# Optimization experiments

Measured on AMD Instinct MI355X. Metric: run time of the kernel, lower is better.

## Reference

```python
import jax, jax.numpy as jnp
import numpy as np

N_QUBITS = 6

def _apply_1q(state, U, w):
    # state: [B] + [2]*6 complex; U: [2,2] complex
    ax = 1 + w
    s = jnp.moveaxis(state, ax, -1)
    s = jnp.einsum('...j,ij->...i', s, U)
    return jnp.moveaxis(s, -1, ax)

def _apply_cnot(state, ctrl, tgt):
    ca, ta = 1 + ctrl, 1 + tgt
    s = jnp.moveaxis(state, (ca, ta), (1, 2))  # [B,2,2,...]
    s = jnp.stack([s[:, 0], s[:, 1, ::-1]], axis=1)
    return jnp.moveaxis(s, (1, 2), (ca, ta))

def _rot(phi, theta, omega):
    # PennyLane Rot = RZ(omega) RY(theta) RZ(phi)
    c, s = jnp.cos(theta / 2), jnp.sin(theta / 2)
    return jnp.stack([
        jnp.stack([jnp.exp(-0.5j * (phi + omega)) * c, -jnp.exp(0.5j * (phi - omega)) * s]),
        jnp.stack([jnp.exp(-0.5j * (phi - omega)) * s, jnp.exp(0.5j * (phi + omega)) * c]),
    ])

def _quantum(xq, qw):
    B = xq.shape[0]
    # AngleEmbedding RY: product state, per-qubit amplitudes [cos(x/2), sin(x/2)]
    amps = jnp.stack([jnp.cos(xq / 2), jnp.sin(xq / 2)], axis=-1)  # [B,6,2]
    state = amps[:, 0]
    for i in range(1, N_QUBITS):
        state = jnp.einsum('b...,bj->b...j', state, amps[:, i])
    state = state.astype(jnp.complex64)  # [B,2,2,2,2,2,2]
    # StronglyEntanglingLayers: per layer Rot on each wire, then CNOT ring of range r
    n_layers = qw.shape[0]
    for l in range(n_layers):
        for w in range(N_QUBITS):
            U = _rot(qw[l, w, 0], qw[l, w, 1], qw[l, w, 2])
            state = _apply_1q(state, U, w)
        r = (l % (N_QUBITS - 1)) + 1  # default ranges
        for w in range(N_QUBITS):
            state = _apply_cnot(state, w, (w + r) % N_QUBITS)
    probs = jnp.abs(state) ** 2
    zs = []
    for w in range(N_QUBITS):
        axes = tuple(a for a in range(1, N_QUBITS + 1) if a != 1 + w)
        p = jnp.sum(probs, axis=axes)  # [B,2]
        zs.append(p[:, 0] - p[:, 1])
    return jnp.stack(zs, axis=-1)  # [B,6]

def setup_inputs() -> dict:
    key = jax.random.key(0)
    ks = jax.random.split(key, 10)
    B = 16384
    return {
        'xc': jax.random.normal(ks[0], (B, 2048), jnp.float32),
        'xq': jax.random.uniform(ks[1], (B, N_QUBITS), jnp.float32),
        'W1': jax.random.normal(ks[2], (64, 2048), jnp.float32) * 0.02,
        'b1': jnp.zeros((64,), jnp.float32),
        'qw': jax.random.uniform(ks[3], (3, N_QUBITS, 3), jnp.float32, 0.0, 2 * np.pi),
        'Wq': jax.random.normal(ks[4], (16, N_QUBITS), jnp.float32) * 0.3,
        'bq': jnp.zeros((16,), jnp.float32),
        'Wf': jax.random.normal(ks[5], (3, 80), jnp.float32) * 0.1,
        'bf': jnp.zeros((3,), jnp.float32),
    }

def reference(xc, xq, W1, b1, qw, Wq, bq, Wf, bf):
    c = jax.nn.relu(xc @ W1.T + b1)                 # [B,64]
    q = _quantum(xq, qw) @ Wq.T + bq                # [B,16]
    return jnp.concatenate([c, q], axis=1) @ Wf.T + bf  # [B,3]
```

## Files before the change

### kernel.cpp

```cpp
#include <hip/hip_runtime.h>
#include <hip/hip_bf16.h>

#define NQ 6

typedef __attribute__((ext_vector_type(8))) short short8;
typedef __attribute__((ext_vector_type(4))) float floatx4;

#define WS_MQ_F   8192
#define WS_CQ_F   (8192+18)
#define WS_W1BF_B 36864

typedef const __attribute__((address_space(1))) void gvoid_t;
typedef __attribute__((address_space(3))) void lvoid_t;

__global__ __launch_bounds__(64) void prep_kernel(
    const float* __restrict__ qw, int n_layers,
    const float* __restrict__ W1, const float* __restrict__ Wq,
    const float* __restrict__ bq, const float* __restrict__ Wf,
    const float* __restrict__ bf, float* __restrict__ ws_f,
    short* __restrict__ w1bf)
{
    const int blk  = blockIdx.x;
    const int lane = threadIdx.x;

    if (blk == 0) {
        if (lane < 18) {
            int j = lane / 6, wi = lane % 6;
            float s = 0.f;
            for (int m = 0; m < 16; ++m) s += Wf[j*80 + 64 + m] * Wq[m*6 + wi];
            ws_f[WS_MQ_F + lane] = s;
        } else if (lane < 21) {
            int j = lane - 18;
            float s = bf[j];
            for (int m = 0; m < 16; ++m) s += Wf[j*80 + 64 + m] * bq[m];
            ws_f[WS_CQ_F + j] = s;
        }
    } else if (blk <= 64) {
        const int j = blk - 1;
        float re = (lane == j) ? 1.f : 0.f;
        float im = 0.f;
        for (int l = 0; l < n_layers; ++l) {
            for (int w = 0; w < NQ; ++w) {
                const float* g = qw + (l*NQ + w)*3;
                float phi = g[0], th = g[1], om = g[2];
                float c, s;  __sincosf(0.5f*th, &s, &c);
                float sa, ca; __sincosf(0.5f*(phi+om), &sa, &ca);
                float sb, cb; __sincosf(0.5f*(phi-om), &sb, &cb);
                float u00r =  c*ca, u00i = -c*sa;
                float u01r = -s*cb, u01i = -s*sb;
                float u10r =  s*cb, u10i = -s*sb;
                float u11r =  c*ca, u11i =  c*sa;
                int p = 5 - w, mask = 1 << p;
                float pre = __shfl_xor(re, mask, 64);
                float pim = __shfl_xor(im, mask, 64);
                int b = (lane >> p) & 1;
                float mr = b ? u11r : u00r, mi = b ? u11i : u00i;
                float pr = b ? u10r : u01r, pi = b ? u10i : u01i;
                float nre = mr*re - mi*im + pr*pre - pi*pim;
                float nim = mr*im + mi*re + pr*pim + pi*pre;
                re = nre; im = nim;
            }
            int r = l % (NQ-1) + 1;
            for (int w = 0; w < NQ; ++w) {
                int tgt = (w + r) % NQ;
                int tmask = 1 << (5 - tgt);
                float pre = __shfl_xor(re, tmask, 64);
                float pim = __shfl_xor(im, tmask, 64);
                int cs = (lane >> (5 - w)) & 1;
                re = cs ? pre : re;
                im = cs ? pim : im;
            }
        }
        ws_f[(lane*64 + j)*2 + 0] = re;
        ws_f[(lane*64 + j)*2 + 1] = im;
    } else {
        int idx = (blk - 65)*512 + lane*8;
        if (idx < 64*2048) {
            float4 a0 = *(const float4*)(W1 + idx);
            float4 a1 = *(const float4*)(W1 + idx + 4);
            union { short8 v; __hip_bfloat162 h[4]; } u;
            float2 f;
            f.x=a0.x; f.y=a0.y; u.h[0] = __float22bfloat162_rn(f);
            f.x=a0.z; f.y=a0.w; u.h[1] = __float22bfloat162_rn(f);
            f.x=a1.x; f.y=a1.y; u.h[2] = __float22bfloat162_rn(f);
            f.x=a1.z; f.y=a1.w; u.h[3] = __float22bfloat162_rn(f);
            *(short8*)(w1bf + idx) = u.v;
        }
    }
}

__device__ __forceinline__ short8 cvt_bf16x8(float4 a0, float4 a1) {
    union { short8 v; __hip_bfloat162 h[4]; } u;
    float2 f;
    f.x=a0.x; f.y=a0.y; u.h[0] = __float22bfloat162_rn(f);
    f.x=a0.z; f.y=a0.w; u.h[1] = __float22bfloat162_rn(f);
    f.x=a1.x; f.y=a1.y; u.h[2] = __float22bfloat162_rn(f);
    f.x=a1.z; f.y=a1.w; u.h[3] = __float22bfloat162_rn(f);
    return u.v;
}

__global__ __launch_bounds__(512, 6) void fused_kernel(
    const float* __restrict__ xq, const float2* __restrict__ U,
    const float* __restrict__ ws_f,
    const float* __restrict__ xc, const short* __restrict__ w1bf,
    const float* __restrict__ b1, const float* __restrict__ Wf,
    float* __restrict__ out)
{
    const int tid  = threadIdx.x;
    const int lane = tid & 63;
    const int t    = __builtin_amdgcn_readfirstlane((int)(tid >> 6));
    const int blk  = blockIdx.x;

    __shared__ __align__(16) char  smem0[16384];
    __shared__ __align__(16) short Bbuf[2][64*128];
    __shared__ float qres[32][3];

    short* Abuf = (short*)smem0;
    float (*zbuf)[32][6] = (float (*)[32][6])smem0;
    float (*cl)[65]      = (float (*)[65])smem0;

    const int wr = t >> 2, wc = t & 3;
    const int srow = tid >> 4;
    const int sgrp = tid & 15;
    const float* asrc = xc + (size_t)(blk*32 + srow)*2048 + sgrp*8;
    const int adoff = srow*128 + ((sgrp ^ (srow & 7)) << 3);
    const int arow = wr*16 + (lane & 15);
    const int abase = arow*128;
    const int arx = arow & 7;
    const int a_l = lane >> 4;
    const int bcol = wc*16 + (lane & 15);
    const int bbase = bcol*128;
    const int brx = bcol & 7;
    const int dc0 = (t*2 + 0)*4 + (lane >> 4);
    const int dc1 = (t*2 + 1)*4 + (lane >> 4);
    const short* bsrc0 = w1bf + dc0*2048 + (((lane & 15) ^ (dc0 & 7)) << 3);
    const short* bsrc1 = w1bf + dc1*2048 + (((lane & 15) ^ (dc1 & 7)) << 3);

    const float* xrow = xq + (size_t)(blk*32 + (lane & 31))*6;
    float2 xq01 = *(const float2*)(xrow);
    float2 xq23 = *(const float2*)(xrow + 2);
    float2 xq45 = *(const float2*)(xrow + 4);

    __builtin_amdgcn_global_load_lds((gvoid_t*)(bsrc0 + 0*128),
        (lvoid_t*)(&Bbuf[0][(t*2+0)*512]), 16, 0, 0);
    __builtin_amdgcn_global_load_lds((gvoid_t*)(bsrc1 + 0*128),
        (lvoid_t*)(&Bbuf[0][(t*2+1)*512]), 16, 0, 0);
    float4 sA0[2], sA1[2];
    sA0[0] = *(const float4*)(asrc + 0*128);
    sA1[0] = *(const float4*)(asrc + 0*128 + 4);

    {
        const float xs[6] = {xq01.x, xq01.y, xq23.x, xq23.y, xq45.x, xq45.y};
        float ah[8], al[8];
        ah[0] = 1.f;
        #pragma unroll
        for (int q = 0; q < 3; ++q) {
            float c, s; __sincosf(0.5f*xs[q], &s, &c);
            const int sz = 1 << q;
            #pragma unroll
            for (int m = sz-1; m >= 0; --m) {
                float v = ah[m];
                ah[2*m+1] = v*s;
                ah[2*m+0] = v*c;
            }
        }
        al[0] = 1.f;
        #pragma unroll
        for (int q = 0; q < 3; ++q) {
            float c, s; __sincosf(0.5f*xs[3+q], &s, &c);
            const int sz = 1 << q;
            #pragma unroll
            for (int m = sz-1; m >= 0; --m) {
                float v = al[m];
                al[2*m+1] = v*s;
                al[2*m+0] = v*c;
            }
        }

        float zp[6] = {0,0,0,0,0,0};
        const float2* Urow = U + t*8*64;
        for (int ii = 0; ii < 8; ++ii) {
            float rr = 0.f, ri = 0.f;
            #pragma unroll
            for (int jh = 0; jh < 8; ++jh) {
                float sr = 0.f, si = 0.f;
                #pragma unroll
                for (int jl = 0; jl < 8; ++jl) {
                    float2 u = Urow[ii*64 + jh*8 + jl];
                    sr += u.x * al[jl];
                    si += u.y * al[jl];
                }
                rr += ah[jh] * sr;
                ri += ah[jh] * si;
            }
            float p = rr*rr + ri*ri;
            int i = t*8 + ii;
            #pragma unroll
            for (int w = 0; w < 6; ++w) zp[w] += ((i >> (5-w)) & 1) ? -p : p;
        }
        if (lane < 32) {
            #pragma unroll
            for (int w = 0; w < 6; ++w) zbuf[t][lane][w] = zp[w];
        }
    }
    __syncthreads();
    if (t == 0 && lane < 32) {
        float z[6];
        #pragma unroll
        for (int w = 0; w < 6; ++w) {
            float s = 0.f;
            #pragma unroll
            for (int sbi = 0; sbi < 8; ++sbi) s += zbuf[sbi][lane][w];
            z[w] = s;
        }
        #pragma unroll
        for (int j = 0; j < 3; ++j) {
            float v = ws_f[WS_CQ_F + j];
            #pragma unroll
            for (int w = 0; w < 6; ++w) v += ws_f[WS_MQ_F + j*6 + w] * z[w];
            qres[lane][j] = v;
        }
    }
    sA0[1] = *(const float4*)(asrc + 1*128);
    sA1[1] = *(const float4*)(asrc + 1*128 + 4);
    __syncthreads();

    *(short8*)(&Abuf[0*4096 + adoff]) = cvt_bf16x8(sA0[0], sA1[0]);
    __syncthreads();

    floatx4 acc = {0,0,0,0};

    #pragma unroll
    for (int c = 0; c < 16; ++c) {
        const int cb = c & 1;

        if (c + 1 < 16) {
            __builtin_amdgcn_global_load_lds((gvoid_t*)(bsrc0 + (c+1)*128),
                (lvoid_t*)(&Bbuf[cb ^ 1][(t*2+0)*512]), 16, 0, 0);
            __builtin_amdgcn_global_load_lds((gvoid_t*)(bsrc1 + (c+1)*128),
                (lvoid_t*)(&Bbuf[cb ^ 1][(t*2+1)*512]), 16, 0, 0);
        }
        if (c + 2 < 16) {
            sA0[cb] = *(const float4*)(asrc + (c+2)*128);
            sA1[cb] = *(const float4*)(asrc + (c+2)*128 + 4);
        }

        const short* abp = &Abuf[cb*4096 + abase];
        const short* bbp = &Bbuf[cb][bbase];
        short8 av0 = *(const short8*)(abp + (((0*4 + a_l) ^ arx) << 3));
        short8 av1 = *(const short8*)(abp + (((1*4 + a_l) ^ arx) << 3));
        short8 av2 = *(const short8*)(abp + (((2*4 + a_l) ^ arx) << 3));
        short8 av3 = *(const short8*)(abp + (((3*4 + a_l) ^ arx) << 3));
        short8 bv0 = *(const short8*)(bbp + (((0*4 + a_l) ^ brx) << 3));
        short8 bv1 = *(const short8*)(bbp + (((1*4 + a_l) ^ brx) << 3));
        short8 bv2 = *(const short8*)(bbp + (((2*4 + a_l) ^ brx) << 3));
        short8 bv3 = *(const short8*)(bbp + (((3*4 + a_l) ^ brx) << 3));
        acc = __builtin_amdgcn_mfma_f32_16x16x32_bf16(av0, bv0, acc, 0, 0, 0);
        acc = __builtin_amdgcn_mfma_f32_16x16x32_bf16(av1, bv1, acc, 0, 0, 0);
        acc = __builtin_amdgcn_mfma_f32_16x16x32_bf16(av2, bv2, acc, 0, 0, 0);
        acc = __builtin_amdgcn_mfma_f32_16x16x32_bf16(av3, bv3, acc, 0, 0, 0);

        if (c + 1 < 16) {
            *(short8*)(&Abuf[(cb ^ 1)*4096 + adoff]) = cvt_bf16x8(sA0[cb ^ 1], sA1[cb ^ 1]);
            __syncthreads();
        }
    }
    __syncthreads();

    const int rbase = wr*16 + a_l*4;
    const float bb = b1[bcol];
    #pragma unroll
    for (int r = 0; r < 4; ++r)
        cl[rbase + r][bcol] = fmaxf(acc[r] + bb, 0.f);
    __syncthreads();

    const int rr2 = lane & 31;
    if (t < 3 && lane < 32) {
        float v = 0.f;
        #pragma unroll
        for (int col = 0; col < 64; ++col) v += Wf[t*80 + col] * cl[rr2][col];
        int g = blk*32 + rr2;
        out[(size_t)g*3 + t] = v + qres[rr2][t];
    }
}

extern "C" void kernel_launch(void* const* d_in, const int* in_sizes, int n_in,
                              void* d_out, int out_size, void* d_ws, size_t ws_size,
                              hipStream_t stream) {
    const float* xc = (const float*)d_in[0];
    const float* xq = (const float*)d_in[1];
    const float* W1 = (const float*)d_in[2];
    const float* b1 = (const float*)d_in[3];
    const float* qw = (const float*)d_in[4];
    const float* Wq = (const float*)d_in[5];
    const float* bq = (const float*)d_in[6];
    const float* Wf = (const float*)d_in[7];
    const float* bf = (const float*)d_in[8];
    float* out = (float*)d_out;

    const int B = in_sizes[1] / NQ;
    const int n_layers = in_sizes[4] / (NQ * 3);

    char* ws = (char*)d_ws;
    float*  ws_f  = (float*)ws;
    float2* U     = (float2*)ws;
    short*  w1bf  = (short*)(ws + WS_W1BF_B);

    prep_kernel<<<dim3(321), dim3(64), 0, stream>>>(qw, n_layers, W1, Wq, bq, Wf, bf, ws_f, w1bf);
    fused_kernel<<<dim3(B/32), dim3(512), 0, stream>>>(xq, U, ws_f, xc, w1bf, b1, Wf, out);
}
```

Measured before the change: 220.9 us.

## Deepen GEMM pipeline to triple-buffered B and three-stage A prefetch with explicit waitcnts

Changes the xc@W1 loop from a double-buffered B tile to three LDS buffers, and prefetches the A-row registers three chunks ahead instead of two. The per-iteration __syncthreads becomes explicit lgkmcnt/vmcnt waits that allow outstanding global loads to stay in flight across the barrier. This is meant to hide more global-memory latency. In exchange it uses more LDS and registers, so launch bounds drop from 6 to 4 blocks per CU, and the hand-counted vmcnt values must match the actual instruction stream to stay correct.

```diff
diff --git a/kernel.cpp b/kernel.cpp
--- a/kernel.cpp
+++ b/kernel.cpp
@@ -99,7 +99,7 @@
     return u.v;
 }
 
-__global__ __launch_bounds__(512, 6) void fused_kernel(
+__global__ __launch_bounds__(512, 4) void fused_kernel(
     const float* __restrict__ xq, const float2* __restrict__ U,
     const float* __restrict__ ws_f,
     const float* __restrict__ xc, const short* __restrict__ w1bf,
@@ -112,7 +112,7 @@
     const int blk  = blockIdx.x;
 
     __shared__ __align__(16) char  smem0[16384];
-    __shared__ __align__(16) short Bbuf[2][64*128];
+    __shared__ __align__(16) short Bbuf[3][64*128];
     __shared__ float qres[32][3];
 
     short* Abuf = (short*)smem0;
@@ -145,9 +145,17 @@
         (lvoid_t*)(&Bbuf[0][(t*2+0)*512]), 16, 0, 0);
     __builtin_amdgcn_global_load_lds((gvoid_t*)(bsrc1 + 0*128),
         (lvoid_t*)(&Bbuf[0][(t*2+1)*512]), 16, 0, 0);
-    float4 sA0[2], sA1[2];
+    __builtin_amdgcn_global_load_lds((gvoid_t*)(bsrc0 + 1*128),
+        (lvoid_t*)(&Bbuf[1][(t*2+0)*512]), 16, 0, 0);
+    __builtin_amdgcn_global_load_lds((gvoid_t*)(bsrc1 + 1*128),
+        (lvoid_t*)(&Bbuf[1][(t*2+1)*512]), 16, 0, 0);
+    float4 sA0[3], sA1[3];
     sA0[0] = *(const float4*)(asrc + 0*128);
     sA1[0] = *(const float4*)(asrc + 0*128 + 4);
+    sA0[1] = *(const float4*)(asrc + 1*128);
+    sA1[1] = *(const float4*)(asrc + 1*128 + 4);
+    sA0[2] = *(const float4*)(asrc + 2*128);
+    sA1[2] = *(const float4*)(asrc + 2*128 + 4);
 
     {
         const float xs[6] = {xq01.x, xq01.y, xq23.x, xq23.y, xq45.x, xq45.y};
@@ -221,8 +229,6 @@
             qres[lane][j] = v;
         }
     }
-    sA0[1] = *(const float4*)(asrc + 1*128);
-    sA1[1] = *(const float4*)(asrc + 1*128 + 4);
     __syncthreads();
 
     *(short8*)(&Abuf[0*4096 + adoff]) = cvt_bf16x8(sA0[0], sA1[0]);
@@ -233,20 +239,24 @@
     #pragma unroll
     for (int c = 0; c < 16; ++c) {
         const int cb = c & 1;
-
-        if (c + 1 < 16) {
-            __builtin_amdgcn_global_load_lds((gvoid_t*)(bsrc0 + (c+1)*128),
-                (lvoid_t*)(&Bbuf[cb ^ 1][(t*2+0)*512]), 16, 0, 0);
-            __builtin_amdgcn_global_load_lds((gvoid_t*)(bsrc1 + (c+1)*128),
-                (lvoid_t*)(&Bbuf[cb ^ 1][(t*2+1)*512]), 16, 0, 0);
-        }
+        const int rb = c % 3;
+
         if (c + 2 < 16) {
-            sA0[cb] = *(const float4*)(asrc + (c+2)*128);
-            sA1[cb] = *(const float4*)(asrc + (c+2)*128 + 4);
+            const int wB = (c + 2) % 3;
+            __builtin_amdgcn_global_load_lds((gvoid_t*)(bsrc0 + (c+2)*128),
+                (lvoid_t*)(&Bbuf[wB][(t*2+0)*512]), 16, 0, 0);
+            __builtin_amdgcn_global_load_lds((gvoid_t*)(bsrc1 + (c+2)*128),
+                (lvoid_t*)(&Bbuf[wB][(t*2+1)*512]), 16, 0, 0);
+        }
+        __builtin_amdgcn_sched_barrier(0);
+        if (c + 3 < 16) {
+            const int sa = c % 3;
+            sA0[sa] = *(const float4*)(asrc + (c+3)*128);
+            sA1[sa] = *(const float4*)(asrc + (c+3)*128 + 4);
         }
 
         const short* abp = &Abuf[cb*4096 + abase];
-        const short* bbp = &Bbuf[cb][bbase];
+        const short* bbp = &Bbuf[rb][bbase];
         short8 av0 = *(const short8*)(abp + (((0*4 + a_l) ^ arx) << 3));
         short8 av1 = *(const short8*)(abp + (((1*4 + a_l) ^ arx) << 3));
         short8 av2 = *(const short8*)(abp + (((2*4 + a_l) ^ arx) << 3));
@@ -261,8 +271,19 @@
         acc = __builtin_amdgcn_mfma_f32_16x16x32_bf16(av3, bv3, acc, 0, 0, 0);
 
         if (c + 1 < 16) {
-            *(short8*)(&Abuf[(cb ^ 1)*4096 + adoff]) = cvt_bf16x8(sA0[cb ^ 1], sA1[cb ^ 1]);
-            __syncthreads();
+            const int fa = (c + 1) % 3;
+            *(short8*)(&Abuf[(cb ^ 1)*4096 + adoff]) = cvt_bf16x8(sA0[fa], sA1[fa]);
+            __builtin_amdgcn_sched_barrier(0);
+            asm volatile("s_waitcnt lgkmcnt(0)" ::: "memory");
+            if (c <= 12) {
+                asm volatile("s_waitcnt vmcnt(6)" ::: "memory");
+            } else if (c == 13) {
+                asm volatile("s_waitcnt vmcnt(4)" ::: "memory");
+            } else {
+                asm volatile("s_waitcnt vmcnt(0)" ::: "memory");
+            }
+            __builtin_amdgcn_s_barrier();
+            __builtin_amdgcn_sched_barrier(0);
         }
     }
     __syncthreads();
```

Result: no change. 221.3 us (+0.2%).

## Stream fp32 A tiles directly to LDS with a triple-buffered async ring

Applied to the files above, without the earlier changes.

The xc activation tile is no longer staged through registers and converted to bf16 before being stored to LDS. Raw fp32 A tiles and bf16 B tiles are now loaded straight into a three-slot LDS ring with global_load_lds, and conversion to bf16 happens at fragment read time. Synchronisation per K-step uses explicit waitcnt and s_barrier, and the K step is halved so there are twice as many iterations. The intent is to drop the register-staging store and deepen prefetch, at the cost of more LDS, fewer blocks per CU (launch bounds lowered from 6 to 4), and conversion work repeated by each wave that reads a fragment.

```diff
diff --git a/kernel.cpp b/kernel.cpp
--- a/kernel.cpp
+++ b/kernel.cpp
@@ -99,7 +99,7 @@
     return u.v;
 }
 
-__global__ __launch_bounds__(512, 6) void fused_kernel(
+__global__ __launch_bounds__(512, 4) void fused_kernel(
     const float* __restrict__ xq, const float2* __restrict__ U,
     const float* __restrict__ ws_f,
     const float* __restrict__ xc, const short* __restrict__ w1bf,
@@ -111,43 +111,42 @@
     const int t    = __builtin_amdgcn_readfirstlane((int)(tid >> 6));
     const int blk  = blockIdx.x;
 
-    __shared__ __align__(16) char  smem0[16384];
-    __shared__ __align__(16) short Bbuf[2][64*128];
+    __shared__ __align__(16) char Aring[3*8192];
+    __shared__ __align__(16) char Bring[3*8192];
+    __shared__ float zbuf[8][32][6];
+    __shared__ float cl[32][65];
     __shared__ float qres[32][3];
 
-    short* Abuf = (short*)smem0;
-    float (*zbuf)[32][6] = (float (*)[32][6])smem0;
-    float (*cl)[65]      = (float (*)[65])smem0;
-
     const int wr = t >> 2, wc = t & 3;
-    const int srow = tid >> 4;
-    const int sgrp = tid & 15;
-    const float* asrc = xc + (size_t)(blk*32 + srow)*2048 + sgrp*8;
-    const int adoff = srow*128 + ((sgrp ^ (srow & 7)) << 3);
+    const int rA = t*4 + (lane >> 4);
+    const int gA = lane & 15;
+    const int uA = gA >> 1;
+    const float* asrcA = xc + (size_t)(blk*32 + rA)*2048
+                       + ((uA ^ (rA & 7)) << 3) + ((gA & 1) << 2);
+    const int colB = t*8 + (lane >> 3);
+    const int gB = lane & 7;
+    const short* bsrcB = w1bf + colB*2048 + ((gB ^ (colB & 7)) << 3);
+    const int a_l  = lane >> 4;
     const int arow = wr*16 + (lane & 15);
-    const int abase = arow*128;
-    const int arx = arow & 7;
-    const int a_l = lane >> 4;
     const int bcol = wc*16 + (lane & 15);
-    const int bbase = bcol*128;
-    const int brx = bcol & 7;
-    const int dc0 = (t*2 + 0)*4 + (lane >> 4);
-    const int dc1 = (t*2 + 1)*4 + (lane >> 4);
-    const short* bsrc0 = w1bf + dc0*2048 + (((lane & 15) ^ (dc0 & 7)) << 3);
-    const short* bsrc1 = w1bf + dc1*2048 + (((lane & 15) ^ (dc1 & 7)) << 3);
+    const int aoff0 = arow*256 + (((0*4 + a_l) ^ (arow & 7)) << 5);
+    const int aoff1 = arow*256 + (((1*4 + a_l) ^ (arow & 7)) << 5);
+    const int boff0 = bcol*128 + (((0*4 + a_l) ^ (bcol & 7)) << 4);
+    const int boff1 = bcol*128 + (((1*4 + a_l) ^ (bcol & 7)) << 4);
 
     const float* xrow = xq + (size_t)(blk*32 + (lane & 31))*6;
     float2 xq01 = *(const float2*)(xrow);
     float2 xq23 = *(const float2*)(xrow + 2);
     float2 xq45 = *(const float2*)(xrow + 4);
 
-    __builtin_amdgcn_global_load_lds((gvoid_t*)(bsrc0 + 0*128),
-        (lvoid_t*)(&Bbuf[0][(t*2+0)*512]), 16, 0, 0);
-    __builtin_amdgcn_global_load_lds((gvoid_t*)(bsrc1 + 0*128),
-        (lvoid_t*)(&Bbuf[0][(t*2+1)*512]), 16, 0, 0);
-    float4 sA0[2], sA1[2];
-    sA0[0] = *(const float4*)(asrc + 0*128);
-    sA1[0] = *(const float4*)(asrc + 0*128 + 4);
+    __builtin_amdgcn_global_load_lds((gvoid_t*)(asrcA + 0*64),
+        (lvoid_t*)(Aring + 0*8192 + t*1024), 16, 0, 0);
+    __builtin_amdgcn_global_load_lds((gvoid_t*)(bsrcB + 0*64),
+        (lvoid_t*)(Bring + 0*8192 + t*1024), 16, 0, 0);
+    __builtin_amdgcn_global_load_lds((gvoid_t*)(asrcA + 1*64),
+        (lvoid_t*)(Aring + 1*8192 + t*1024), 16, 0, 0);
+    __builtin_amdgcn_global_load_lds((gvoid_t*)(bsrcB + 1*64),
+        (lvoid_t*)(Bring + 1*8192 + t*1024), 16, 0, 0);
 
     {
         const float xs[6] = {xq01.x, xq01.y, xq23.x, xq23.y, xq45.x, xq45.y};
@@ -221,57 +220,52 @@
             qres[lane][j] = v;
         }
     }
-    sA0[1] = *(const float4*)(asrc + 1*128);
-    sA1[1] = *(const float4*)(asrc + 1*128 + 4);
     __syncthreads();
 
-    *(short8*)(&Abuf[0*4096 + adoff]) = cvt_bf16x8(sA0[0], sA1[0]);
+    floatx4 acc = {0,0,0,0};
+
+    #pragma unroll
+    for (int c = 0; c < 32; ++c) {
+        const int rs = c % 3;
+
+        if (c + 2 < 32) {
+            const int wslot = (c + 2) % 3;
+            __builtin_amdgcn_global_load_lds((gvoid_t*)(asrcA + (c+2)*64),
+                (lvoid_t*)(Aring + wslot*8192 + t*1024), 16, 0, 0);
+            __builtin_amdgcn_global_load_lds((gvoid_t*)(bsrcB + (c+2)*64),
+                (lvoid_t*)(Bring + wslot*8192 + t*1024), 16, 0, 0);
+        }
+
+        const char* ab = Aring + rs*8192;
+        const char* bb = Bring + rs*8192;
+        float4 f00 = *(const float4*)(ab + aoff0);
+        float4 f01 = *(const float4*)(ab + aoff0 + 16);
+        float4 f10 = *(const float4*)(ab + aoff1);
+        float4 f11 = *(const float4*)(ab + aoff1 + 16);
+        short8 bv0 = *(const short8*)(bb + boff0);
+        short8 bv1 = *(const short8*)(bb + boff1);
+        acc = __builtin_amdgcn_mfma_f32_16x16x32_bf16(cvt_bf16x8(f00, f01), bv0, acc, 0, 0, 0);
+        acc = __builtin_amdgcn_mfma_f32_16x16x32_bf16(cvt_bf16x8(f10, f11), bv1, acc, 0, 0, 0);
+
+        if (c < 31) {
+            __builtin_amdgcn_sched_barrier(0);
+            asm volatile("s_waitcnt lgkmcnt(0)" ::: "memory");
+            if (c <= 29) {
+                asm volatile("s_waitcnt vmcnt(2)" ::: "memory");
+            } else {
+                asm volatile("s_waitcnt vmcnt(0)" ::: "memory");
+            }
+            __builtin_amdgcn_s_barrier();
+            __builtin_amdgcn_sched_barrier(0);
+        }
+    }
     __syncthreads();
 
-    floatx4 acc = {0,0,0,0};
-
-    #pragma unroll
-    for (int c = 0; c < 16; ++c) {
-        const int cb = c & 1;
-
-        if (c + 1 < 16) {
-            __builtin_amdgcn_global_load_lds((gvoid_t*)(bsrc0 + (c+1)*128),
-                (lvoid_t*)(&Bbuf[cb ^ 1][(t*2+0)*512]), 16, 0, 0);
-            __builtin_amdgcn_global_load_lds((gvoid_t*)(bsrc1 + (c+1)*128),
-                (lvoid_t*)(&Bbuf[cb ^ 1][(t*2+1)*512]), 16, 0, 0);
-        }
-        if (c + 2 < 16) {
-            sA0[cb] = *(const float4*)(asrc + (c+2)*128);
-            sA1[cb] = *(const float4*)(asrc + (c+2)*128 + 4);
-        }
-
-        const short* abp = &Abuf[cb*4096 + abase];
-        const short* bbp = &Bbuf[cb][bbase];
-        short8 av0 = *(const short8*)(abp + (((0*4 + a_l) ^ arx) << 3));
-        short8 av1 = *(const short8*)(abp + (((1*4 + a_l) ^ arx) << 3));
-        short8 av2 = *(const short8*)(abp + (((2*4 + a_l) ^ arx) << 3));
-        short8 av3 = *(const short8*)(abp + (((3*4 + a_l) ^ arx) << 3));
-        short8 bv0 = *(const short8*)(bbp + (((0*4 + a_l) ^ brx) << 3));
-        short8 bv1 = *(const short8*)(bbp + (((1*4 + a_l) ^ brx) << 3));
-        short8 bv2 = *(const short8*)(bbp + (((2*4 + a_l) ^ brx) << 3));
-        short8 bv3 = *(const short8*)(bbp + (((3*4 + a_l) ^ brx) << 3));
-        acc = __builtin_amdgcn_mfma_f32_16x16x32_bf16(av0, bv0, acc, 0, 0, 0);
-        acc = __builtin_amdgcn_mfma_f32_16x16x32_bf16(av1, bv1, acc, 0, 0, 0);
-        acc = __builtin_amdgcn_mfma_f32_16x16x32_bf16(av2, bv2, acc, 0, 0, 0);
-        acc = __builtin_amdgcn_mfma_f32_16x16x32_bf16(av3, bv3, acc, 0, 0, 0);
-
-        if (c + 1 < 16) {
-            *(short8*)(&Abuf[(cb ^ 1)*4096 + adoff]) = cvt_bf16x8(sA0[cb ^ 1], sA1[cb ^ 1]);
-            __syncthreads();
-        }
-    }
-    __syncthreads();
-
     const int rbase = wr*16 + a_l*4;
-    const float bb = b1[bcol];
+    const float bb1 = b1[bcol];
     #pragma unroll
     for (int r = 0; r < 4; ++r)
-        cl[rbase + r][bcol] = fmaxf(acc[r] + bb, 0.f);
+        cl[rbase + r][bcol] = fmaxf(acc[r] + bb1, 0.f);
     __syncthreads();
 
     const int rr2 = lane & 31;
```

New measurement: 237.6 us. +7.5%, slower.
